# Kernel tuning notes

Measured on AMD Instinct MI355X. Metric: run time of the kernel, lower is better.

## Reference

```python
import jax, jax.numpy as jnp
from jax import lax
import numpy as np

NPOINT, RADIUS, NSAMPLE = 1024, 0.2, 32
MLP, IN_CH, EPS = (64, 64, 128), 6, 1e-5
B, N = 8, 4096


def farthest_point_sample(xyz, npoint):
    # xyz: [B, N, 3] -> idx [B, npoint]. Deterministic start at index 0.
    Bn, Nn, _ = xyz.shape
    def body(carry, _):
        dist, farthest = carry  # dist [B,N], farthest [B]
        centroid = jnp.take_along_axis(xyz, farthest[:, None, None], axis=1)  # [B,1,3]
        d = jnp.sum((xyz - centroid) ** 2, axis=-1)  # [B,N]
        dist = jnp.minimum(dist, d)
        return (dist, jnp.argmax(dist, axis=-1).astype(jnp.int32)), farthest
    init = (jnp.full((Bn, Nn), 1e10, xyz.dtype), jnp.zeros((Bn,), jnp.int32))
    _, idx = lax.scan(body, init, None, length=npoint)  # [npoint, B]
    return idx.T


def query_ball_point(radius, nsample, xyz, new_xyz):
    # xyz [B,N,3], new_xyz [B,S,3] -> idx [B,S,nsample]
    Bn, Nn, _ = xyz.shape
    sq = (jnp.sum(new_xyz ** 2, -1)[:, :, None]
          + jnp.sum(xyz ** 2, -1)[:, None, :]
          - 2.0 * jnp.einsum('bsc,bnc->bsn', new_xyz, xyz))  # [B,S,N]
    gidx = jnp.where(sq > radius ** 2, Nn, jnp.arange(Nn, dtype=jnp.int32)[None, None, :])
    gidx = jnp.sort(gidx, axis=-1)[:, :, :nsample]
    first = gidx[:, :, :1]
    return jnp.where(gidx == Nn, first, gidx)


def setup_inputs():
    key = jax.random.key(0)
    ks = jax.random.split(key, 8)
    inp = {
        'xyz': jax.random.uniform(ks[0], (B, 3, N), dtype=jnp.float32),
        'points': jax.random.normal(ks[1], (B, 3, N), dtype=jnp.float32),
    }
    last = IN_CH
    for i, oc in enumerate(MLP):
        inp[f'w{i}'] = jax.random.normal(ks[2 + i], (oc, last), dtype=jnp.float32) * 0.1
        inp[f'b{i}'] = jnp.zeros((oc,), jnp.float32)
        inp[f'g{i}'] = jnp.ones((oc,), jnp.float32)
        inp[f'be{i}'] = jnp.zeros((oc,), jnp.float32)
        last = oc
    return inp


def reference(xyz, points, w0, b0, g0, be0, w1, b1, g1, be1, w2, b2, g2, be2):
    x = jnp.transpose(xyz, (0, 2, 1))      # [B,N,3]
    p = jnp.transpose(points, (0, 2, 1))   # [B,N,D]
    fidx = farthest_point_sample(x, NPOINT)                       # [B,S]
    new_xyz = jnp.take_along_axis(x, fidx[:, :, None], axis=1)    # [B,S,3]
    idx = query_ball_point(RADIUS, NSAMPLE, x, new_xyz)           # [B,S,K]
    gather = jax.vmap(lambda a, i: a[i])                          # per-batch gather
    grouped_xyz = gather(x, idx)                                  # [B,S,K,3]
    grouped_xyz_norm = grouped_xyz - new_xyz[:, :, None, :]
    grouped_points = gather(p, idx)                               # [B,S,K,D]
    feat = jnp.concatenate([grouped_xyz_norm, grouped_points], axis=-1)  # [B,S,K,C]
    for w, b, g, be in ((w0, b0, g0, be0), (w1, b1, g1, be1), (w2, b2, g2, be2)):
        feat = jnp.einsum('bskc,oc->bsko', feat, w) + b
        mean = feat.mean(axis=(0, 1, 2))
        var = feat.var(axis=(0, 1, 2))
        feat = (feat - mean) * lax.rsqrt(var + EPS) * g + be  # BatchNorm (training stats)
        feat = jax.nn.relu(feat)
    new_points = jnp.max(feat, axis=2)                            # max over K -> [B,S,Cout]
    return jnp.transpose(new_xyz, (0, 2, 1)), jnp.transpose(new_points, (0, 2, 1))
```

## Files before the change

kernel.cpp:

```cpp
#include <hip/hip_runtime.h>
#include <stdint.h>

#define NPTS   4096
#define NPOINT 1024
#define NSAMP  32
#define NROWS  262144
#define RAD2   0.04f

typedef float v2f __attribute__((ext_vector_type(2)));
typedef __attribute__((ext_vector_type(8))) short bf16x8;
typedef __attribute__((ext_vector_type(4))) float f32x4;

__device__ __forceinline__ unsigned short f2bf(float x) {
    unsigned u = __float_as_uint(x);
    return (unsigned short)((u + 0x7FFFu + ((u >> 16) & 1u)) >> 16);
}
__device__ __forceinline__ unsigned pack2bf(float a, float b) {
    return (unsigned)f2bf(a) | ((unsigned)f2bf(b) << 16);
}

__global__ __launch_bounds__(256) void fps_kernel(const float* __restrict__ xyz,
                                                  float* __restrict__ outx)
{
    __shared__ __align__(16) float4 pxyz[NPTS];
    __shared__ __align__(16) float4 orec[NPOINT];
    __shared__ __align__(16) unsigned long long wkey[2][4];
    __shared__ __align__(16) float4 wxyz[2][4];
    const int b = blockIdx.x, tid = threadIdx.x;
    const int lane = tid & 63, wid = tid >> 6;
    const float* base = xyz + b * 3 * NPTS;

    float Xs[16], Ys[16], Zs[16];
#pragma unroll
    for (int j = 0; j < 16; ++j) {
        const int n = j * 256 + tid;
        Xs[j] = base[n];
        Ys[j] = base[NPTS + n];
        Zs[j] = base[2 * NPTS + n];
        pxyz[n] = make_float4(Xs[j], Ys[j], Zs[j], 0.0f);
    }
    v2f X2[8], Y2[8], Z2[8], D2[8];
#pragma unroll
    for (int j = 0; j < 8; ++j) {
        X2[j] = (v2f){Xs[2 * j], Xs[2 * j + 1]};
        Y2[j] = (v2f){Ys[2 * j], Ys[2 * j + 1]};
        Z2[j] = (v2f){Zs[2 * j], Zs[2 * j + 1]};
        D2[j] = (v2f){1e10f, 1e10f};
    }
    __syncthreads();
    float4 c4 = pxyz[0];
    float cx = c4.x, cy = c4.y, cz = c4.z;

    for (int t = 0; t < NPOINT; ++t) {
        if (tid == (t & 255)) orec[t] = make_float4(cx, cy, cz, 0.0f);
        const v2f cxv = (v2f){cx, cx}, cyv = (v2f){cy, cy}, czv = (v2f){cz, cz};
        float bv = -1.0f; int bi = 0;
#pragma unroll
        for (int j = 0; j < 8; ++j) {
            v2f nd;
            {
#pragma clang fp contract(off)
                const v2f dx = X2[j] - cxv;
                const v2f dy = Y2[j] - cyv;
                const v2f dz = Z2[j] - czv;
                const v2f m0 = dx * dx;
                const v2f m1 = dy * dy;
                const v2f m2 = dz * dz;
                const v2f d = (m0 + m1) + m2;
                nd = __builtin_elementwise_min(D2[j], d);
            }
            D2[j] = nd;
            if (nd.x > bv) { bv = nd.x; bi = j * 512 + tid; }
            if (nd.y > bv) { bv = nd.y; bi = j * 512 + 256 + tid; }
        }
        unsigned kv = __float_as_uint(bv);
        unsigned ki = ~(unsigned)bi;
#define DPP_STEP(C)                                                            \
        {                                                                      \
            unsigned ov = (unsigned)__builtin_amdgcn_update_dpp(               \
                0, (int)kv, C, 0xf, 0xf, true);                                \
            unsigned oi = (unsigned)__builtin_amdgcn_update_dpp(               \
                0, (int)ki, C, 0xf, 0xf, true);                                \
            bool g = (ov > kv) || (ov == kv && oi > ki);                       \
            kv = g ? ov : kv;                                                  \
            ki = g ? oi : ki;                                                  \
        }
        DPP_STEP(0x111)
        DPP_STEP(0x112)
        DPP_STEP(0x114)
        DPP_STEP(0x118)
        DPP_STEP(0x142)
        DPP_STEP(0x143)
#undef DPP_STEP
        const unsigned wv = (unsigned)__builtin_amdgcn_readlane((int)kv, 63);
        const unsigned wi = (unsigned)__builtin_amdgcn_readlane((int)ki, 63);
        const int widx = (int)(~wi) & (NPTS - 1);
        const float4 wc4 = pxyz[widx];
        if (lane == 0) {
            wkey[t & 1][wid] = ((unsigned long long)wv << 32) | wi;
            wxyz[t & 1][wid] = wc4;
        }
        __syncthreads();
        const ulonglong2* wk = (const ulonglong2*)wkey[t & 1];
        const float4* wc = wxyz[t & 1];
        const ulonglong2 ka = wk[0], kb = wk[1];
        const float4 c0 = wc[0], c1 = wc[1], c2 = wc[2], c3 = wc[3];
        const bool gA = ka.y > ka.x;
        const unsigned long long k01 = gA ? ka.y : ka.x;
        const bool gB = kb.y > kb.x;
        const unsigned long long k23 = gB ? kb.y : kb.x;
        const float4 c01 = gA ? c1 : c0;
        const float4 c23 = gB ? c3 : c2;
        const bool gg = k23 > k01;
        cx = gg ? c23.x : c01.x;
        cy = gg ? c23.y : c01.y;
        cz = gg ? c23.z : c01.z;
    }
    __syncthreads();
    float* ox = outx + b * 3 * NPOINT;
    for (int i = tid; i < NPOINT; i += 256) {
        const float4 c = orec[i];
        ox[i]              = c.x;
        ox[NPOINT + i]     = c.y;
        ox[2 * NPOINT + i] = c.z;
    }
}

__global__ __launch_bounds__(256) void ball_kernel(const float* __restrict__ xyz,
                                                   const float* __restrict__ outx,
                                                   int* __restrict__ idxbuf)
{
    const int w = blockIdx.x * 4 + (threadIdx.x >> 6);
    const int lane = threadIdx.x & 63;
    const int b = w >> 10, s = w & 1023;
    const float* base = xyz + b * 3 * NPTS;
    const float cx = outx[b * 3 * NPOINT + s];
    const float cy = outx[b * 3 * NPOINT + NPOINT + s];
    const float cz = outx[b * 3 * NPOINT + 2 * NPOINT + s];
    const float sumS = __fadd_rn(__fadd_rn(__fmul_rn(cx, cx), __fmul_rn(cy, cy)),
                                 __fmul_rn(cz, cz));
    int cnt = 0, first_n = -1;
    int* myidx = idxbuf + w * NSAMP;

    for (int chunk = 0; chunk < NPTS / 64 && cnt < NSAMP; ++chunk) {
        const int n = chunk * 64 + lane;
        float nx = base[n], ny = base[NPTS + n], nz = base[2 * NPTS + n];
        float sumN = __fadd_rn(__fadd_rn(__fmul_rn(nx, nx), __fmul_rn(ny, ny)),
                               __fmul_rn(nz, nz));
        float dot = __fadd_rn(__fadd_rn(__fmul_rn(cx, nx), __fmul_rn(cy, ny)),
                              __fmul_rn(cz, nz));
        float sq = __fsub_rn(__fadd_rn(sumS, sumN), __fmul_rn(2.0f, dot));
        bool keep = (sq <= RAD2);
        unsigned long long mask = __ballot(keep);
        if (first_n < 0 && mask) first_n = chunk * 64 + (int)__builtin_ctzll(mask);
        int pos = cnt + __popcll(mask & ((1ull << lane) - 1ull));
        if (keep && pos < NSAMP) myidx[pos] = n;
        cnt += __popcll(mask);
    }
    if (cnt < NSAMP) {
        if (lane >= cnt && lane < NSAMP) myidx[lane] = first_n;
    }
}

__device__ __forceinline__ void load_feats(const float* __restrict__ xyz,
                                           const float* __restrict__ pts,
                                           const float* __restrict__ outx,
                                           int r, int idx, float f[6])
{
    const int b = r >> 15;
    const int s = (r >> 5) & 1023;
    const float* xb = xyz + b * 3 * NPTS;
    const float* pb = pts + b * 3 * NPTS;
    const float* ob = outx + b * 3 * NPOINT;
    f[0] = xb[idx] - ob[s];
    f[1] = xb[NPTS + idx] - ob[NPOINT + s];
    f[2] = xb[2 * NPTS + idx] - ob[2 * NPOINT + s];
    f[3] = pb[idx];
    f[4] = pb[NPTS + idx];
    f[5] = pb[2 * NPTS + idx];
}

__global__ __launch_bounds__(256, 2) void mom_kernel(
    const float* __restrict__ xyz, const float* __restrict__ pts,
    const float* __restrict__ outx, const int* __restrict__ idxbuf,
    float* __restrict__ mom)
{
    __shared__ float red[4][42];
    const int tid = threadIdx.x, lane = tid & 63, wid = tid >> 6;
    float m[42];
#pragma unroll
    for (int i = 0; i < 42; ++i) m[i] = 0.f;
    const int r0 = blockIdx.x * 1024 + tid;
#pragma unroll
    for (int k = 0; k < 4; ++k) {
        const int r = r0 + k * 256;
        float f[6];
        load_feats(xyz, pts, outx, r, idxbuf[r], f);
#pragma unroll
        for (int c = 0; c < 6; ++c) m[c] += f[c];
#pragma unroll
        for (int c = 0; c < 6; ++c)
#pragma unroll
            for (int d = 0; d < 6; ++d)
                m[6 + c * 6 + d] = fmaf(f[c], f[d], m[6 + c * 6 + d]);
    }
#pragma unroll
    for (int i = 0; i < 42; ++i) {
        float v = m[i];
        v += __shfl_xor(v, 1);  v += __shfl_xor(v, 2);  v += __shfl_xor(v, 4);
        v += __shfl_xor(v, 8);  v += __shfl_xor(v, 16); v += __shfl_xor(v, 32);
        m[i] = v;
    }
    if (lane == 0) {
#pragma unroll
        for (int i = 0; i < 42; ++i) red[wid][i] = m[i];
    }
    __syncthreads();
    if (tid < 42)
        atomicAdd(&mom[tid], red[0][tid] + red[1][tid] + red[2][tid] + red[3][tid]);
}

__global__ void bnparam0_kernel(const float* __restrict__ mom,
                                const float* __restrict__ w0,
                                const float* __restrict__ g,
                                const float* __restrict__ be,
                                float* __restrict__ bn)
{
    const int o = threadIdx.x;
    float w[6];
#pragma unroll
    for (int c = 0; c < 6; ++c) w[c] = w0[o * 6 + c];
    const float inv = 1.0f / (float)NROWS;
    float mean = 0.f;
#pragma unroll
    for (int c = 0; c < 6; ++c) mean = fmaf(w[c], mom[c], mean);
    mean *= inv;
    float ey2 = 0.f;
#pragma unroll
    for (int c = 0; c < 6; ++c) {
        float t = 0.f;
#pragma unroll
        for (int d = 0; d < 6; ++d) t = fmaf(w[d], mom[6 + c * 6 + d], t);
        ey2 = fmaf(w[c], t, ey2);
    }
    ey2 *= inv;
    const float var = ey2 - mean * mean;
    const float scale = g[o] * rsqrtf(var + 1e-5f);
    bn[o] = scale;
    bn[64 + o] = be[o] - mean * scale;
}

__global__ void bnparam_kernel(const float* __restrict__ stats,
                               const float* __restrict__ g,
                               const float* __restrict__ be,
                               float* __restrict__ bn, int C)
{
    const int t = threadIdx.x;
    if (t >= C) return;
    const float inv = 1.0f / (float)NROWS;
    float mean = stats[t] * inv;
    float var = stats[C + t] * inv - mean * mean;
    float scale = g[t] * rsqrtf(var + 1e-5f);
    bn[t] = scale;
    bn[C + t] = be[t] - mean * scale;
}

#define XP  72
#define WP  72
#define W0P 40

__global__ __launch_bounds__(256, 2) void mlp1_kernel(
    const float* __restrict__ xyz, const float* __restrict__ pts,
    const float* __restrict__ outx, const int* __restrict__ idxbuf,
    const float* __restrict__ w0, const float* __restrict__ bn0,
    const float* __restrict__ w1, float* __restrict__ stats)
{
    __shared__ __align__(16) unsigned short sw0[64 * W0P];
    __shared__ __align__(16) unsigned short sw1[64 * WP];
    __shared__ __align__(16) unsigned short xb[4][32 * XP];
    __shared__ float sbn0[128];
    __shared__ float red[4][128];
    const int tid = threadIdx.x, lane = tid & 63, wid = tid >> 6;

    for (int i = tid; i < 64 * W0P / 2; i += 256) ((unsigned*)sw0)[i] = 0;
    if (tid < 128) sbn0[tid] = bn0[tid];
    __syncthreads();
    for (int i = tid; i < 192; i += 256) {
        const int o = i / 3, c = (i % 3) * 2;
        *(unsigned*)&sw0[o * W0P + c] = pack2bf(w0[o * 6 + c], w0[o * 6 + c + 1]);
    }
    for (int i = tid; i < 2048; i += 256) {
        const int o = i >> 5, k = (i & 31) * 2;
        *(unsigned*)&sw1[o * WP + k] = pack2bf(w1[o * 64 + k], w1[o * 64 + k + 1]);
    }

    const int mh = lane & 15, q = lane >> 4;
    unsigned short* X = xb[wid];
    const int rbase = blockIdx.x * 512 + wid * 32;
    float sA[4] = {0.f, 0.f, 0.f, 0.f}, qA[4] = {0.f, 0.f, 0.f, 0.f};

    for (int c = 0; c < 4; ++c) {
        __syncthreads();
        if (lane < 32) {
            const int r = rbase + c * 128 + lane;
            float f[6];
            load_feats(xyz, pts, outx, r, idxbuf[r], f);
            uint4* xq = (uint4*)&xb[wid][lane * XP];
            xq[0] = make_uint4(pack2bf(f[0], f[1]), pack2bf(f[2], f[3]),
                               pack2bf(f[4], f[5]), 0u);
            xq[1] = make_uint4(0u, 0u, 0u, 0u);
            xq[2] = make_uint4(0u, 0u, 0u, 0u);
            xq[3] = make_uint4(0u, 0u, 0u, 0u);
        }
        __syncthreads();
        f32x4 acc0[2][4] = {};
        {
            bf16x8 a[2], bw[4];
#pragma unroll
            for (int mt = 0; mt < 2; ++mt)
                a[mt] = *(const bf16x8*)&X[(mt * 16 + mh) * XP + q * 8];
#pragma unroll
            for (int nt = 0; nt < 4; ++nt)
                bw[nt] = *(const bf16x8*)&sw0[(nt * 16 + mh) * W0P + q * 8];
#pragma unroll
            for (int mt = 0; mt < 2; ++mt)
#pragma unroll
                for (int nt = 0; nt < 4; ++nt)
                    acc0[mt][nt] = __builtin_amdgcn_mfma_f32_16x16x32_bf16(
                        a[mt], bw[nt], acc0[mt][nt], 0, 0, 0);
        }
        __syncthreads();
#pragma unroll
        for (int nt = 0; nt < 4; ++nt) {
            const int ch = nt * 16 + mh;
            const float sc = sbn0[ch], sh = sbn0[64 + ch];
#pragma unroll
            for (int mt = 0; mt < 2; ++mt)
#pragma unroll
                for (int rr = 0; rr < 4; ++rr) {
                    const float v = fmaxf(fmaf(acc0[mt][nt][rr], sc, sh), 0.0f);
                    X[(mt * 16 + q * 4 + rr) * XP + ch] = f2bf(v);
                }
        }
        __syncthreads();
        f32x4 acc1[2][4] = {};
#pragma unroll
        for (int ks = 0; ks < 2; ++ks) {
            bf16x8 a[2], bw[4];
#pragma unroll
            for (int mt = 0; mt < 2; ++mt)
                a[mt] = *(const bf16x8*)&X[(mt * 16 + mh) * XP + ks * 32 + q * 8];
#pragma unroll
            for (int nt = 0; nt < 4; ++nt)
                bw[nt] = *(const bf16x8*)&sw1[(nt * 16 + mh) * WP + ks * 32 + q * 8];
#pragma unroll
            for (int mt = 0; mt < 2; ++mt)
#pragma unroll
                for (int nt = 0; nt < 4; ++nt)
                    acc1[mt][nt] = __builtin_amdgcn_mfma_f32_16x16x32_bf16(
                        a[mt], bw[nt], acc1[mt][nt], 0, 0, 0);
        }
#pragma unroll
        for (int nt = 0; nt < 4; ++nt)
#pragma unroll
            for (int mt = 0; mt < 2; ++mt)
#pragma unroll
                for (int rr = 0; rr < 4; ++rr) {
                    const float v = acc1[mt][nt][rr];
                    sA[nt] += v;
                    qA[nt] = fmaf(v, v, qA[nt]);
                }
    }
#pragma unroll
    for (int nt = 0; nt < 4; ++nt) {
        float s = sA[nt], qq = qA[nt];
        s += __shfl_xor(s, 16); qq += __shfl_xor(qq, 16);
        s += __shfl_xor(s, 32); qq += __shfl_xor(qq, 32);
        if (q == 0) {
            red[wid][nt * 16 + mh] = s;
            red[wid][64 + nt * 16 + mh] = qq;
        }
    }
    __syncthreads();
    if (tid < 128)
        atomicAdd(&stats[tid],
                  red[0][tid] + red[1][tid] + red[2][tid] + red[3][tid]);
}

__global__ __launch_bounds__(256, 2) void mlp2_kernel(
    const float* __restrict__ xyz, const float* __restrict__ pts,
    const float* __restrict__ outx, const int* __restrict__ idxbuf,
    const float* __restrict__ w0, const float* __restrict__ bn0,
    const float* __restrict__ w1, const float* __restrict__ bn1,
    const float* __restrict__ w2,
    float* __restrict__ stats, float* __restrict__ gmax)
{
    __shared__ __align__(16) unsigned short sw0[64 * W0P];
    __shared__ __align__(16) unsigned short sw1[64 * WP];
    __shared__ __align__(16) unsigned short sw2[128 * WP];
    __shared__ __align__(16) unsigned short xb[4][32 * XP];
    __shared__ float sbn0[128];
    __shared__ float sbn1[128];
    __shared__ float red[4][256];
    const int tid = threadIdx.x, lane = tid & 63, wid = tid >> 6;

    for (int i = tid; i < 64 * W0P / 2; i += 256) ((unsigned*)sw0)[i] = 0;
    if (tid < 128) { sbn0[tid] = bn0[tid]; sbn1[tid] = bn1[tid]; }
    __syncthreads();
    for (int i = tid; i < 192; i += 256) {
        const int o = i / 3, c = (i % 3) * 2;
        *(unsigned*)&sw0[o * W0P + c] = pack2bf(w0[o * 6 + c], w0[o * 6 + c + 1]);
    }
    for (int i = tid; i < 2048; i += 256) {
        const int o = i >> 5, k = (i & 31) * 2;
        *(unsigned*)&sw1[o * WP + k] = pack2bf(w1[o * 64 + k], w1[o * 64 + k + 1]);
    }
    for (int i = tid; i < 4096; i += 256) {
        const int o = i >> 5, k = (i & 31) * 2;
        *(unsigned*)&sw2[o * WP + k] = pack2bf(w2[o * 64 + k], w2[o * 64 + k + 1]);
    }

    const int mh = lane & 15, q = lane >> 4;
    unsigned short* X = xb[wid];
    const int rbase = blockIdx.x * 512 + wid * 32;
    float sA[8], qA[8];
#pragma unroll
    for (int i = 0; i < 8; ++i) { sA[i] = 0.f; qA[i] = 0.f; }

    for (int c = 0; c < 4; ++c) {
        __syncthreads();
        if (lane < 32) {
            const int r = rbase + c * 128 + lane;
            float f[6];
            load_feats(xyz, pts, outx, r, idxbuf[r], f);
            uint4* xq = (uint4*)&xb[wid][lane * XP];
            xq[0] = make_uint4(pack2bf(f[0], f[1]), pack2bf(f[2], f[3]),
                               pack2bf(f[4], f[5]), 0u);
            xq[1] = make_uint4(0u, 0u, 0u, 0u);
            xq[2] = make_uint4(0u, 0u, 0u, 0u);
            xq[3] = make_uint4(0u, 0u, 0u, 0u);
        }
        __syncthreads();
        f32x4 acc0[2][4] = {};
        {
            bf16x8 a[2], bw[4];
#pragma unroll
            for (int mt = 0; mt < 2; ++mt)
                a[mt] = *(const bf16x8*)&X[(mt * 16 + mh) * XP + q * 8];
#pragma unroll
            for (int nt = 0; nt < 4; ++nt)
                bw[nt] = *(const bf16x8*)&sw0[(nt * 16 + mh) * W0P + q * 8];
#pragma unroll
            for (int mt = 0; mt < 2; ++mt)
#pragma unroll
                for (int nt = 0; nt < 4; ++nt)
                    acc0[mt][nt] = __builtin_amdgcn_mfma_f32_16x16x32_bf16(
                        a[mt], bw[nt], acc0[mt][nt], 0, 0, 0);
        }
        __syncthreads();
#pragma unroll
        for (int nt = 0; nt < 4; ++nt) {
            const int ch = nt * 16 + mh;
            const float sc = sbn0[ch], sh = sbn0[64 + ch];
#pragma unroll
            for (int mt = 0; mt < 2; ++mt)
#pragma unroll
                for (int rr = 0; rr < 4; ++rr) {
                    const float v = fmaxf(fmaf(acc0[mt][nt][rr], sc, sh), 0.0f);
                    X[(mt * 16 + q * 4 + rr) * XP + ch] = f2bf(v);
                }
        }
        __syncthreads();
        f32x4 acc1[2][4] = {};
#pragma unroll
        for (int ks = 0; ks < 2; ++ks) {
            bf16x8 a[2], bw[4];
#pragma unroll
            for (int mt = 0; mt < 2; ++mt)
                a[mt] = *(const bf16x8*)&X[(mt * 16 + mh) * XP + ks * 32 + q * 8];
#pragma unroll
            for (int nt = 0; nt < 4; ++nt)
                bw[nt] = *(const bf16x8*)&sw1[(nt * 16 + mh) * WP + ks * 32 + q * 8];
#pragma unroll
            for (int mt = 0; mt < 2; ++mt)
#pragma unroll
                for (int nt = 0; nt < 4; ++nt)
                    acc1[mt][nt] = __builtin_amdgcn_mfma_f32_16x16x32_bf16(
                        a[mt], bw[nt], acc1[mt][nt], 0, 0, 0);
        }
        __syncthreads();
#pragma unroll
        for (int nt = 0; nt < 4; ++nt) {
            const int ch = nt * 16 + mh;
            const float sc = sbn1[ch], sh = sbn1[64 + ch];
#pragma unroll
            for (int mt = 0; mt < 2; ++mt)
#pragma unroll
                for (int rr = 0; rr < 4; ++rr) {
                    const float v = fmaxf(fmaf(acc1[mt][nt][rr], sc, sh), 0.0f);
                    X[(mt * 16 + q * 4 + rr) * XP + ch] = f2bf(v);
                }
        }
        __syncthreads();
        const int g = blockIdx.x * 16 + c * 4 + wid;
        bf16x8 a2[2][2];
#pragma unroll
        for (int mt = 0; mt < 2; ++mt)
#pragma unroll
            for (int ks = 0; ks < 2; ++ks)
                a2[mt][ks] = *(const bf16x8*)&X[(mt * 16 + mh) * XP + ks * 32 + q * 8];
#pragma unroll
        for (int nt = 0; nt < 8; ++nt) {
            f32x4 acc[2] = {};
#pragma unroll
            for (int ks = 0; ks < 2; ++ks) {
                const bf16x8 bw = *(const bf16x8*)&sw2[(nt * 16 + mh) * WP + ks * 32 + q * 8];
#pragma unroll
                for (int mt = 0; mt < 2; ++mt)
                    acc[mt] = __builtin_amdgcn_mfma_f32_16x16x32_bf16(
                        a2[mt][ks], bw, acc[mt], 0, 0, 0);
            }
            float m = -3.0e38f;
#pragma unroll
            for (int mt = 0; mt < 2; ++mt)
#pragma unroll
                for (int rr = 0; rr < 4; ++rr) {
                    const float v = acc[mt][rr];
                    sA[nt] += v;
                    qA[nt] = fmaf(v, v, qA[nt]);
                    m = fmaxf(m, v);
                }
            m = fmaxf(m, __shfl_xor(m, 16));
            m = fmaxf(m, __shfl_xor(m, 32));
            if (q == 0) gmax[(nt * 16 + mh) * 8192 + g] = m;
        }
    }
#pragma unroll
    for (int nt = 0; nt < 8; ++nt) {
        float s = sA[nt], qq = qA[nt];
        s += __shfl_xor(s, 16); qq += __shfl_xor(qq, 16);
        s += __shfl_xor(s, 32); qq += __shfl_xor(qq, 32);
        if (q == 0) {
            red[wid][nt * 16 + mh] = s;
            red[wid][128 + nt * 16 + mh] = qq;
        }
    }
    __syncthreads();
    atomicAdd(&stats[tid],
              red[0][tid] + red[1][tid] + red[2][tid] + red[3][tid]);
}

__global__ __launch_bounds__(256) void final_kernel(const float* __restrict__ gmax,
                                                    const float* __restrict__ bn2,
                                                    float* __restrict__ out2)
{
    const int t = blockIdx.x * 256 + threadIdx.x;
    const int s = t & 1023;
    const int o = (t >> 10) & 127;
    const int b = t >> 17;
    const int g = (b << 10) | s;
    float v = gmax[o * 8192 + g];
    v = fmaf(v, bn2[o], bn2[128 + o]);
    out2[t] = fmaxf(v, 0.0f);
}

extern "C" void kernel_launch(void* const* d_in, const int* in_sizes, int n_in,
                              void* d_out, int out_size, void* d_ws, size_t ws_size,
                              hipStream_t stream)
{
    const float* xyz = (const float*)d_in[0];
    const float* pts = (const float*)d_in[1];
    const float* w0  = (const float*)d_in[2];
    const float* g0  = (const float*)d_in[4];
    const float* be0 = (const float*)d_in[5];
    const float* w1  = (const float*)d_in[6];
    const float* g1  = (const float*)d_in[8];
    const float* be1 = (const float*)d_in[9];
    const float* w2  = (const float*)d_in[10];
    const float* g2  = (const float*)d_in[12];
    const float* be2 = (const float*)d_in[13];

    float* out_xyz = (float*)d_out;
    float* out2    = out_xyz + 8 * 3 * NPOINT;

    char* wsb = (char*)d_ws;
    int*   idxbuf = (int*)(wsb + 32768);
    float* stats  = (float*)(wsb + 32768 + 1048576);
    float* bnp    = stats + 512;
    float* gmax   = bnp + 512;

    float* mom    = stats;
    float* stats1 = stats + 128; float* stats2 = stats + 256;
    float* bn0    = bnp;         float* bn1    = bnp + 128;   float* bn2 = bnp + 256;

    hipMemsetAsync(stats, 0, 512 * sizeof(float), stream);

    fps_kernel<<<8, 256, 0, stream>>>(xyz, out_xyz);
    ball_kernel<<<2048, 256, 0, stream>>>(xyz, out_xyz, idxbuf);
    mom_kernel<<<256, 256, 0, stream>>>(xyz, pts, out_xyz, idxbuf, mom);
    bnparam0_kernel<<<1, 64, 0, stream>>>(mom, w0, g0, be0, bn0);
    mlp1_kernel<<<512, 256, 0, stream>>>(xyz, pts, out_xyz, idxbuf, w0, bn0, w1, stats1);
    bnparam_kernel<<<1, 64, 0, stream>>>(stats1, g1, be1, bn1, 64);
    mlp2_kernel<<<512, 256, 0, stream>>>(xyz, pts, out_xyz, idxbuf, w0, bn0, w1, bn1, w2, stats2, gmax);
    bnparam_kernel<<<1, 128, 0, stream>>>(stats2, g2, be2, bn2, 128);
    final_kernel<<<4096, 256, 0, stream>>>(gmax, bn2, out2);
}
```

Measured before the change: 866.0 us.

## Simplify FPS argmax reduction and fuse moment and BN-param kernels into neighbors

The FPS argmax now does a float max reduction followed by a min-index reduction instead of a paired key/index DPP compare. The winning point is looked up from LDS after the barrier, so each wave no longer publishes its candidate coordinates. The moment accumulation moves into the ball-query kernel, and the BN parameter computations are folded into the prologues of mlp1, mlp2 and the final kernel. This removes four launches (mom and three bnparam) and their serialization gaps. In exchange it adds redundant per-block BN parameter math, 2048-way atomics on the moments, and an extra dependent LDS read in the FPS critical loop.

Result: faster. 808.6 us (-6.6%).

```diff
diff --git a/kernel.cpp b/kernel.cpp
--- a/kernel.cpp
+++ b/kernel.cpp
@@ -19,13 +19,21 @@
     return (unsigned)f2bf(a) | ((unsigned)f2bf(b) << 16);
 }
 
+#define DPPMAX(v, C)                                                           \
+    fmaxf(__int_as_float(__builtin_amdgcn_update_dpp(                          \
+              0, __float_as_int(v), C, 0xf, 0xf, true)),                       \
+          (v))
+#define DPPMIN(v, C)                                                           \
+    ({ unsigned _o = (unsigned)__builtin_amdgcn_update_dpp(                    \
+           -1, (int)(v), C, 0xf, 0xf, false);                                  \
+       (_o < (v)) ? _o : (v); })
+
 __global__ __launch_bounds__(256) void fps_kernel(const float* __restrict__ xyz,
                                                   float* __restrict__ outx)
 {
     __shared__ __align__(16) float4 pxyz[NPTS];
     __shared__ __align__(16) float4 orec[NPOINT];
     __shared__ __align__(16) unsigned long long wkey[2][4];
-    __shared__ __align__(16) float4 wxyz[2][4];
     const int b = blockIdx.x, tid = threadIdx.x;
     const int lane = tid & 63, wid = tid >> 6;
     const float* base = xyz + b * 3 * NPTS;
@@ -52,7 +60,7 @@
     float cx = c4.x, cy = c4.y, cz = c4.z;
 
     for (int t = 0; t < NPOINT; ++t) {
-        if (tid == (t & 255)) orec[t] = make_float4(cx, cy, cz, 0.0f);
+        if (tid == 0) orec[t] = make_float4(cx, cy, cz, 0.0f);
         const v2f cxv = (v2f){cx, cx}, cyv = (v2f){cy, cy}, czv = (v2f){cz, cz};
         float bv = -1.0f; int bi = 0;
 #pragma unroll
@@ -73,48 +81,36 @@
             if (nd.x > bv) { bv = nd.x; bi = j * 512 + tid; }
             if (nd.y > bv) { bv = nd.y; bi = j * 512 + 256 + tid; }
         }
-        unsigned kv = __float_as_uint(bv);
-        unsigned ki = ~(unsigned)bi;
-#define DPP_STEP(C)                                                            \
-        {                                                                      \
-            unsigned ov = (unsigned)__builtin_amdgcn_update_dpp(               \
-                0, (int)kv, C, 0xf, 0xf, true);                                \
-            unsigned oi = (unsigned)__builtin_amdgcn_update_dpp(               \
-                0, (int)ki, C, 0xf, 0xf, true);                                \
-            bool g = (ov > kv) || (ov == kv && oi > ki);                       \
-            kv = g ? ov : kv;                                                  \
-            ki = g ? oi : ki;                                                  \
-        }
-        DPP_STEP(0x111)
-        DPP_STEP(0x112)
-        DPP_STEP(0x114)
-        DPP_STEP(0x118)
-        DPP_STEP(0x142)
-        DPP_STEP(0x143)
-#undef DPP_STEP
-        const unsigned wv = (unsigned)__builtin_amdgcn_readlane((int)kv, 63);
-        const unsigned wi = (unsigned)__builtin_amdgcn_readlane((int)ki, 63);
-        const int widx = (int)(~wi) & (NPTS - 1);
-        const float4 wc4 = pxyz[widx];
-        if (lane == 0) {
-            wkey[t & 1][wid] = ((unsigned long long)wv << 32) | wi;
-            wxyz[t & 1][wid] = wc4;
-        }
+        float rv = bv;
+        rv = DPPMAX(rv, 0x111);
+        rv = DPPMAX(rv, 0x112);
+        rv = DPPMAX(rv, 0x114);
+        rv = DPPMAX(rv, 0x118);
+        rv = DPPMAX(rv, 0x142);
+        rv = DPPMAX(rv, 0x143);
+        const unsigned wmax =
+            (unsigned)__builtin_amdgcn_readlane(__float_as_int(rv), 63);
+        unsigned cand = (__float_as_uint(bv) == wmax) ? (unsigned)bi
+                                                      : 0xFFFFFFFFu;
+        cand = DPPMIN(cand, 0x111);
+        cand = DPPMIN(cand, 0x112);
+        cand = DPPMIN(cand, 0x114);
+        cand = DPPMIN(cand, 0x118);
+        cand = DPPMIN(cand, 0x142);
+        cand = DPPMIN(cand, 0x143);
+        if (lane == 63)
+            wkey[t & 1][wid] = ((unsigned long long)wmax << 32) |
+                               (unsigned)(~cand);
         __syncthreads();
         const ulonglong2* wk = (const ulonglong2*)wkey[t & 1];
-        const float4* wc = wxyz[t & 1];
         const ulonglong2 ka = wk[0], kb = wk[1];
-        const float4 c0 = wc[0], c1 = wc[1], c2 = wc[2], c3 = wc[3];
-        const bool gA = ka.y > ka.x;
-        const unsigned long long k01 = gA ? ka.y : ka.x;
-        const bool gB = kb.y > kb.x;
-        const unsigned long long k23 = gB ? kb.y : kb.x;
-        const float4 c01 = gA ? c1 : c0;
-        const float4 c23 = gB ? c3 : c2;
-        const bool gg = k23 > k01;
-        cx = gg ? c23.x : c01.x;
-        cy = gg ? c23.y : c01.y;
-        cz = gg ? c23.z : c01.z;
+        unsigned long long kk = ka.x;
+        if (ka.y > kk) kk = ka.y;
+        if (kb.x > kk) kk = kb.x;
+        if (kb.y > kk) kk = kb.y;
+        const int farthest = (int)(~(unsigned)kk) & (NPTS - 1);
+        c4 = pxyz[farthest];
+        cx = c4.x; cy = c4.y; cz = c4.z;
     }
     __syncthreads();
     float* ox = outx + b * 3 * NPOINT;
@@ -127,11 +123,15 @@
 }
 
 __global__ __launch_bounds__(256) void ball_kernel(const float* __restrict__ xyz,
+                                                   const float* __restrict__ pts,
                                                    const float* __restrict__ outx,
-                                                   int* __restrict__ idxbuf)
-{
-    const int w = blockIdx.x * 4 + (threadIdx.x >> 6);
-    const int lane = threadIdx.x & 63;
+                                                   int* __restrict__ idxbuf,
+                                                   float* __restrict__ mom)
+{
+    __shared__ float red[4][42];
+    const int tid = threadIdx.x;
+    const int w = blockIdx.x * 4 + (tid >> 6);
+    const int lane = tid & 63, wid = tid >> 6;
     const int b = w >> 10, s = w & 1023;
     const float* base = xyz + b * 3 * NPTS;
     const float cx = outx[b * 3 * NPOINT + s];
@@ -160,6 +160,42 @@
     if (cnt < NSAMP) {
         if (lane >= cnt && lane < NSAMP) myidx[lane] = first_n;
     }
+
+    float m[42];
+#pragma unroll
+    for (int i = 0; i < 42; ++i) m[i] = 0.f;
+    if (lane < 32) {
+        const int idx = myidx[lane];
+        const float* pb = pts + b * 3 * NPTS;
+        float f[6];
+        f[0] = base[idx] - cx;
+        f[1] = base[NPTS + idx] - cy;
+        f[2] = base[2 * NPTS + idx] - cz;
+        f[3] = pb[idx];
+        f[4] = pb[NPTS + idx];
+        f[5] = pb[2 * NPTS + idx];
+#pragma unroll
+        for (int c = 0; c < 6; ++c) m[c] = f[c];
+#pragma unroll
+        for (int c = 0; c < 6; ++c)
+#pragma unroll
+            for (int d = 0; d < 6; ++d)
+                m[6 + c * 6 + d] = f[c] * f[d];
+    }
+#pragma unroll
+    for (int i = 0; i < 42; ++i) {
+        float v = m[i];
+        v += __shfl_xor(v, 1);  v += __shfl_xor(v, 2);  v += __shfl_xor(v, 4);
+        v += __shfl_xor(v, 8);  v += __shfl_xor(v, 16); v += __shfl_xor(v, 32);
+        m[i] = v;
+    }
+    if (lane == 0) {
+#pragma unroll
+        for (int i = 0; i < 42; ++i) red[wid][i] = m[i];
+    }
+    __syncthreads();
+    if (tid < 42)
+        atomicAdd(&mom[tid], red[0][tid] + red[1][tid] + red[2][tid] + red[3][tid]);
 }
 
 __device__ __forceinline__ void load_feats(const float* __restrict__ xyz,
@@ -180,53 +216,12 @@
     f[5] = pb[2 * NPTS + idx];
 }
 
-__global__ __launch_bounds__(256, 2) void mom_kernel(
-    const float* __restrict__ xyz, const float* __restrict__ pts,
-    const float* __restrict__ outx, const int* __restrict__ idxbuf,
-    float* __restrict__ mom)
-{
-    __shared__ float red[4][42];
-    const int tid = threadIdx.x, lane = tid & 63, wid = tid >> 6;
-    float m[42];
-#pragma unroll
-    for (int i = 0; i < 42; ++i) m[i] = 0.f;
-    const int r0 = blockIdx.x * 1024 + tid;
-#pragma unroll
-    for (int k = 0; k < 4; ++k) {
-        const int r = r0 + k * 256;
-        float f[6];
-        load_feats(xyz, pts, outx, r, idxbuf[r], f);
-#pragma unroll
-        for (int c = 0; c < 6; ++c) m[c] += f[c];
-#pragma unroll
-        for (int c = 0; c < 6; ++c)
-#pragma unroll
-            for (int d = 0; d < 6; ++d)
-                m[6 + c * 6 + d] = fmaf(f[c], f[d], m[6 + c * 6 + d]);
-    }
-#pragma unroll
-    for (int i = 0; i < 42; ++i) {
-        float v = m[i];
-        v += __shfl_xor(v, 1);  v += __shfl_xor(v, 2);  v += __shfl_xor(v, 4);
-        v += __shfl_xor(v, 8);  v += __shfl_xor(v, 16); v += __shfl_xor(v, 32);
-        m[i] = v;
-    }
-    if (lane == 0) {
-#pragma unroll
-        for (int i = 0; i < 42; ++i) red[wid][i] = m[i];
-    }
-    __syncthreads();
-    if (tid < 42)
-        atomicAdd(&mom[tid], red[0][tid] + red[1][tid] + red[2][tid] + red[3][tid]);
-}
-
-__global__ void bnparam0_kernel(const float* __restrict__ mom,
-                                const float* __restrict__ w0,
-                                const float* __restrict__ g,
-                                const float* __restrict__ be,
-                                float* __restrict__ bn)
-{
-    const int o = threadIdx.x;
+__device__ __forceinline__ void compute_bn0(int o, const float* __restrict__ mom,
+                                            const float* __restrict__ w0,
+                                            const float* __restrict__ g,
+                                            const float* __restrict__ be,
+                                            float* __restrict__ sbn0)
+{
     float w[6];
 #pragma unroll
     for (int c = 0; c < 6; ++c) w[c] = w0[o * 6 + c];
@@ -246,23 +241,8 @@
     ey2 *= inv;
     const float var = ey2 - mean * mean;
     const float scale = g[o] * rsqrtf(var + 1e-5f);
-    bn[o] = scale;
-    bn[64 + o] = be[o] - mean * scale;
-}
-
-__global__ void bnparam_kernel(const float* __restrict__ stats,
-                               const float* __restrict__ g,
-                               const float* __restrict__ be,
-                               float* __restrict__ bn, int C)
-{
-    const int t = threadIdx.x;
-    if (t >= C) return;
-    const float inv = 1.0f / (float)NROWS;
-    float mean = stats[t] * inv;
-    float var = stats[C + t] * inv - mean * mean;
-    float scale = g[t] * rsqrtf(var + 1e-5f);
-    bn[t] = scale;
-    bn[C + t] = be[t] - mean * scale;
+    sbn0[o] = scale;
+    sbn0[64 + o] = be[o] - mean * scale;
 }
 
 #define XP  72
@@ -272,7 +252,8 @@
 __global__ __launch_bounds__(256, 2) void mlp1_kernel(
     const float* __restrict__ xyz, const float* __restrict__ pts,
     const float* __restrict__ outx, const int* __restrict__ idxbuf,
-    const float* __restrict__ w0, const float* __restrict__ bn0,
+    const float* __restrict__ w0, const float* __restrict__ mom,
+    const float* __restrict__ g0, const float* __restrict__ be0,
     const float* __restrict__ w1, float* __restrict__ stats)
 {
     __shared__ __align__(16) unsigned short sw0[64 * W0P];
@@ -283,7 +264,7 @@
     const int tid = threadIdx.x, lane = tid & 63, wid = tid >> 6;
 
     for (int i = tid; i < 64 * W0P / 2; i += 256) ((unsigned*)sw0)[i] = 0;
-    if (tid < 128) sbn0[tid] = bn0[tid];
+    if (tid < 64) compute_bn0(tid, mom, w0, g0, be0, sbn0);
     __syncthreads();
     for (int i = tid; i < 192; i += 256) {
         const int o = i / 3, c = (i % 3) * 2;
@@ -390,8 +371,10 @@
 __global__ __launch_bounds__(256, 2) void mlp2_kernel(
     const float* __restrict__ xyz, const float* __restrict__ pts,
     const float* __restrict__ outx, const int* __restrict__ idxbuf,
-    const float* __restrict__ w0, const float* __restrict__ bn0,
-    const float* __restrict__ w1, const float* __restrict__ bn1,
+    const float* __restrict__ w0, const float* __restrict__ mom,
+    const float* __restrict__ g0, const float* __restrict__ be0,
+    const float* __restrict__ w1, const float* __restrict__ stats1,
+    const float* __restrict__ g1, const float* __restrict__ be1,
     const float* __restrict__ w2,
     float* __restrict__ stats, float* __restrict__ gmax)
 {
@@ -405,7 +388,17 @@
     const int tid = threadIdx.x, lane = tid & 63, wid = tid >> 6;
 
     for (int i = tid; i < 64 * W0P / 2; i += 256) ((unsigned*)sw0)[i] = 0;
-    if (tid < 128) { sbn0[tid] = bn0[tid]; sbn1[tid] = bn1[tid]; }
+    if (tid < 64) {
+        compute_bn0(tid, mom, w0, g0, be0, sbn0);
+    } else if (tid < 128) {
+        const int ch = tid - 64;
+        const float inv = 1.0f / (float)NROWS;
+        const float mean = stats1[ch] * inv;
+        const float var = stats1[64 + ch] * inv - mean * mean;
+        const float scale = g1[ch] * rsqrtf(var + 1e-5f);
+        sbn1[ch] = scale;
+        sbn1[64 + ch] = be1[ch] - mean * scale;
+    }
     __syncthreads();
     for (int i = tid; i < 192; i += 256) {
         const int o = i / 3, c = (i % 3) * 2;
@@ -551,16 +544,29 @@
 }
 
 __global__ __launch_bounds__(256) void final_kernel(const float* __restrict__ gmax,
-                                                    const float* __restrict__ bn2,
+                                                    const float* __restrict__ stats2,
+                                                    const float* __restrict__ g2,
+                                                    const float* __restrict__ be2,
                                                     float* __restrict__ out2)
 {
-    const int t = blockIdx.x * 256 + threadIdx.x;
+    __shared__ float sbn[256];
+    const int tid = threadIdx.x;
+    if (tid < 128) {
+        const float inv = 1.0f / (float)NROWS;
+        const float mean = stats2[tid] * inv;
+        const float var = stats2[128 + tid] * inv - mean * mean;
+        const float scale = g2[tid] * rsqrtf(var + 1e-5f);
+        sbn[tid] = scale;
+        sbn[128 + tid] = be2[tid] - mean * scale;
+    }
+    __syncthreads();
+    const int t = blockIdx.x * 256 + tid;
     const int s = t & 1023;
     const int o = (t >> 10) & 127;
     const int b = t >> 17;
     const int g = (b << 10) | s;
     float v = gmax[o * 8192 + g];
-    v = fmaf(v, bn2[o], bn2[128 + o]);
+    v = fmaf(v, sbn[o], sbn[128 + o]);
     out2[t] = fmaxf(v, 0.0f);
 }
 
@@ -586,22 +592,20 @@
     char* wsb = (char*)d_ws;
     int*   idxbuf = (int*)(wsb + 32768);
     float* stats  = (float*)(wsb + 32768 + 1048576);
-    float* bnp    = stats + 512;
-    float* gmax   = bnp + 512;
+    float* gmax   = stats + 1024;
 
     float* mom    = stats;
-    float* stats1 = stats + 128; float* stats2 = stats + 256;
-    float* bn0    = bnp;         float* bn1    = bnp + 128;   float* bn2 = bnp + 256;
+    float* stats1 = stats + 128;
+    float* stats2 = stats + 256;
 
     hipMemsetAsync(stats, 0, 512 * sizeof(float), stream);
 
     fps_kernel<<<8, 256, 0, stream>>>(xyz, out_xyz);
-    ball_kernel<<<2048, 256, 0, stream>>>(xyz, out_xyz, idxbuf);
-    mom_kernel<<<256, 256, 0, stream>>>(xyz, pts, out_xyz, idxbuf, mom);
-    bnparam0_kernel<<<1, 64, 0, stream>>>(mom, w0, g0, be0, bn0);
-    mlp1_kernel<<<512, 256, 0, stream>>>(xyz, pts, out_xyz, idxbuf, w0, bn0, w1, stats1);
-    bnparam_kernel<<<1, 64, 0, stream>>>(stats1, g1, be1, bn1, 64);
-    mlp2_kernel<<<512, 256, 0, stream>>>(xyz, pts, out_xyz, idxbuf, w0, bn0, w1, bn1, w2, stats2, gmax);
-    bnparam_kernel<<<1, 128, 0, stream>>>(stats2, g2, be2, bn2, 128);
-    final_kernel<<<4096, 256, 0, stream>>>(gmax, bn2, out2);
-}
+    ball_kernel<<<2048, 256, 0, stream>>>(xyz, pts, out_xyz, idxbuf, mom);
+    mlp1_kernel<<<512, 256, 0, stream>>>(xyz, pts, out_xyz, idxbuf,
+                                         w0, mom, g0, be0, w1, stats1);
+    mlp2_kernel<<<512, 256, 0, stream>>>(xyz, pts, out_xyz, idxbuf,
+                                         w0, mom, g0, be0, w1, stats1, g1, be1,
+                                         w2, stats2, gmax);
+    final_kernel<<<4096, 256, 0, stream>>>(gmax, stats2, g2, be2, out2);
+}
```
